# Kernel tuning notes

Measured on AMD Instinct MI355X. Metric: run time of the kernel, lower is better.

The kernel has to match this reference:

```python
import jax, jax.numpy as jnp
import numpy as np

E, T, H, I = 16, 4, 512, 1024  # expert_num, task_num, hidden_size, input_size
B = 8192


def setup_inputs() -> dict:
    key = jax.random.key(0)
    ks = jax.random.split(key, 8)
    s_i = 1.0 / np.sqrt(I)
    s_h = 1.0 / np.sqrt(H)
    return {
        "x": jax.random.normal(ks[0], (B, I), dtype=jnp.float32),
        "We": jax.random.uniform(ks[1], (E, H, I), jnp.float32, -s_i, s_i),
        "be": jax.random.uniform(ks[2], (E, H), jnp.float32, -s_i, s_i),
        "Wg": jax.random.uniform(ks[3], (T, E, I), jnp.float32, -s_i, s_i),
        "bg": jax.random.uniform(ks[4], (T, E), jnp.float32, -s_i, s_i),
        "Wf": jax.random.uniform(ks[5], (T, H), jnp.float32, -s_h, s_h),
        "bf": jax.random.uniform(ks[6], (T,), jnp.float32, -s_h, s_h),
    }


def reference(x, We, be, Wg, bg, Wf, bf):
    # expert outputs: relu(x @ We_e^T + be_e)  -> [B, E, H]
    eo = jax.nn.relu(jnp.einsum("bi,ehi->beh", x, We) + be[None])
    # gate outputs: softmax over experts        -> [B, T, E]
    g = jax.nn.softmax(jnp.einsum("bi,tei->bte", x, Wg) + bg[None], axis=-1)
    # gated combine                             -> [T, B, H]
    res = jnp.einsum("bte,beh->tbh", g, eo)
    # per-task scalar heads                     -> [T, B, 1]
    out = jnp.einsum("tbh,th->tb", res, Wf) + bf[:, None]
    return out[:, :, None]
```

## Files before the change

kernel.cpp:

```cpp
#include <hip/hip_runtime.h>
#include <hip/hip_bf16.h>
#include <stdint.h>


#define E_ 16
#define T_ 4
#define H_ 512
#define I_ 1024
#define B_ 8192
#define N_ (E_ * H_)
#define K_ I_

typedef __bf16 bf16x8 __attribute__((ext_vector_type(8)));
typedef float f32x4 __attribute__((ext_vector_type(4)));

__device__ __forceinline__ unsigned short f2bf_rne(float f) {
  unsigned int b = __float_as_uint(f);
  b += 0x7fffu + ((b >> 16) & 1u);
  return (unsigned short)(b >> 16);
}

#define N4X (B_ * K_ / 4)
#define N4W (N_ * K_ / 4)
#define N4G (64 * K_ / 4)

__global__ __launch_bounds__(256) void cvt3_kernel(const float* __restrict__ x,
                                                   const float* __restrict__ We,
                                                   const float* __restrict__ Wg,
                                                   const float* __restrict__ bfv,
                                                   unsigned short* __restrict__ xb,
                                                   unsigned short* __restrict__ wb,
                                                   unsigned short* __restrict__ wgb,
                                                   float* __restrict__ out) {
  int i = blockIdx.x * 256 + threadIdx.x;
  if (i < T_ * B_) out[i] = bfv[i >> 13];
  const float* src;
  unsigned short* dst;
  int j;
  if (i < N4X) {
    src = x; dst = xb; j = i;
  } else if (i < N4X + N4W) {
    src = We; dst = wb; j = i - N4X;
  } else if (i < N4X + N4W + N4G) {
    src = Wg; dst = wgb; j = i - (N4X + N4W);
  } else {
    return;
  }
  float4 v = reinterpret_cast<const float4*>(src)[j];
  ushort4 o;
  o.x = f2bf_rne(v.x);
  o.y = f2bf_rne(v.y);
  o.z = f2bf_rne(v.z);
  o.w = f2bf_rne(v.w);
  reinterpret_cast<ushort4*>(dst)[j] = o;
}

__device__ __forceinline__ void gld_lds16(const void* gp, void* lp) {
  __builtin_amdgcn_global_load_lds((const __attribute__((address_space(1))) void*)gp,
                                   (__attribute__((address_space(3))) void*)lp, 16, 0, 0);
}

__global__ __launch_bounds__(256) void logits_softmax_kernel(
    const unsigned short* __restrict__ A,
    const unsigned short* __restrict__ Bm,
    const float* __restrict__ bg,
    float* __restrict__ g)
{
  __shared__ struct {
    unsigned short A[128 * 32];
    unsigned short B[64 * 32];
  } st;

  const int tid = threadIdx.x;
  const int w = tid >> 6, l = tid & 63;
  const int m16 = l & 15, q = l >> 4;
  const size_t m0 = (size_t)blockIdx.x * 128;

  const int r0s = (w * 2 + 0) * 16 + (l >> 2);
  const int r1s = (w * 2 + 1) * 16 + (l >> 2);
  const int slot = l & 3;
  const int c0 = slot ^ ((r0s >> 1) & 3);
  const int c1 = slot ^ ((r1s >> 1) & 3);
  const size_t offA0 = (m0 + r0s) * K_ + c0 * 8;
  const size_t offA1 = (m0 + r1s) * K_ + c1 * 8;
  const int l0 = (w * 2 + 0) * 512;
  const int l1 = (w * 2 + 1) * 512;
  const int rBs = w * 16 + (l >> 2);
  const int cB = slot ^ ((rBs >> 1) & 3);
  const size_t offB = (size_t)rBs * K_ + cB * 8;
  const int lB = w * 512;

  const int arow = w * 32 + m16;
  const int sA = q ^ ((arow >> 1) & 3);
  const int sB = q ^ ((m16 >> 1) & 3);

  f32x4 acc[2][4] = {};

  for (int k0 = 0; k0 < K_; k0 += 32) {
    __syncthreads();
    gld_lds16(A + offA0 + k0, st.A + l0);
    gld_lds16(A + offA1 + k0, st.A + l1);
    gld_lds16(Bm + offB + k0, st.B + lB);
    __syncthreads();
    bf16x8 af[2], bfr[4];
#pragma unroll
    for (int i = 0; i < 2; ++i)
      af[i] = *reinterpret_cast<const bf16x8*>(st.A + (arow + i * 16) * 32 + sA * 8);
#pragma unroll
    for (int j = 0; j < 4; ++j)
      bfr[j] = *reinterpret_cast<const bf16x8*>(st.B + (j * 16 + m16) * 32 + sB * 8);
#pragma unroll
    for (int i = 0; i < 2; ++i)
#pragma unroll
      for (int j = 0; j < 4; ++j)
        acc[i][j] = __builtin_amdgcn_mfma_f32_16x16x32_bf16(af[i], bfr[j], acc[i][j], 0, 0, 0);
  }

  float bgv[4];
#pragma unroll
  for (int j = 0; j < 4; ++j) bgv[j] = bg[j * 16 + m16];

#pragma unroll
  for (int i = 0; i < 2; ++i) {
    float lg[4][4];
#pragma unroll
    for (int j = 0; j < 4; ++j)
#pragma unroll
      for (int r = 0; r < 4; ++r) lg[r][j] = acc[i][j][r] + bgv[j];
#pragma unroll
    for (int r = 0; r < 4; ++r) {
#pragma unroll
      for (int j = 0; j < 4; ++j) {
        float m = lg[r][j];
#pragma unroll
        for (int mask = 1; mask < 16; mask <<= 1) m = fmaxf(m, __shfl_xor(m, mask, 64));
        float ex = __expf(lg[r][j] - m);
        float s = ex;
#pragma unroll
        for (int mask = 1; mask < 16; mask <<= 1) s += __shfl_xor(s, mask, 64);
        size_t b = m0 + w * 32 + i * 16 + q * 4 + r;
        g[b * 64 + j * 16 + m16] = ex / s;
      }
    }
  }
}


extern __shared__ char smem[];

#define BARRIER()                          \
  do {                                     \
    asm volatile("" ::: "memory");         \
    __builtin_amdgcn_s_barrier();          \
    asm volatile("" ::: "memory");         \
  } while (0)
#define VMW(n) asm volatile("s_waitcnt vmcnt(" #n ")" ::: "memory")
#define LGKM(n) asm volatile("s_waitcnt lgkmcnt(" #n ")" ::: "memory")
#define SCHED0() __builtin_amdgcn_sched_barrier(0)

#define STAGE4(t_)                                                             \
  do {                                                                         \
    const int bb_ = ((t_) & 3) * 32768;                                        \
    const int ko_ = (t_) * 32;                                                 \
    gld_lds16(A + baseAg + ko_, smem + bb_ + ldsW);                            \
    gld_lds16(A + baseAg + 16 * K_ + ko_, smem + bb_ + ldsW + 1024);           \
    gld_lds16(Bm + baseBg + ko_, smem + bb_ + 16384 + ldsW);                   \
    gld_lds16(Bm + baseBg + 16 * K_ + ko_, smem + bb_ + 16384 + ldsW + 1024);  \
  } while (0)

#define READF(S, t_)                                                                      \
  do {                                                                                    \
    const int bb_ = ((t_) & 3) * 32768;                                                   \
    _Pragma("unroll") for (int i = 0; i < 8; ++i) af##S[i] =                              \
        *reinterpret_cast<const bf16x8*>(smem + bb_ + baseA_rd + i * 1024 + sl16);        \
    _Pragma("unroll") for (int j = 0; j < 4; ++j) bfr##S[j] =                             \
        *reinterpret_cast<const bf16x8*>(smem + bb_ + 16384 + baseB_rd + j * 1024 + sl16);\
  } while (0)

#define MFMA32(S)                                                                         \
  do {                                                                                    \
    __builtin_amdgcn_s_setprio(1);                                                        \
    _Pragma("unroll") for (int i = 0; i < 8; ++i)                                         \
        _Pragma("unroll") for (int j = 0; j < 4; ++j)                                     \
            acc[i][j] = __builtin_amdgcn_mfma_f32_16x16x32_bf16(af##S[i], bfr##S[j],      \
                                                                acc[i][j], 0, 0, 0);      \
    __builtin_amdgcn_s_setprio(0);                                                        \
    SCHED0();                                                                             \
  } while (0)

__global__ __launch_bounds__(512, 2) void moe_main_kernel(
    const unsigned short* __restrict__ A,
    const unsigned short* __restrict__ Bm,
    const float* __restrict__ be,
    const float* __restrict__ Wf,
    const float* __restrict__ g,
    float* __restrict__ out)
{
  const int tid = threadIdx.x;
  const int w = tid >> 6, l = tid & 63;
  const int wm = w >> 2, wn = w & 3;
  const int m16 = l & 15, q = l >> 4;
  const int mb = blockIdx.x, nb = blockIdx.y;
  const size_t m0 = (size_t)mb * 256, n0 = (size_t)nb * 256;

  const int c8 = (((l & 3) ^ ((l >> 3) & 3)) * 8);
  const size_t baseAg = (m0 + w * 32 + (l >> 2)) * K_ + c8;
  const size_t baseBg = (n0 + w * 32 + (l >> 2)) * K_ + c8;
  const int ldsW = w * 2048;

  const int sl16 = (q ^ ((m16 >> 1) & 3)) * 16;
  const int baseA_rd = (wm * 128 + m16) * 64;
  const int baseB_rd = (wn * 64 + m16) * 64;

  f32x4 acc[8][4] = {};
  bf16x8 afA[8], bfrA[4], afB[8], bfrB[4];

  STAGE4(0);
  STAGE4(1);
  STAGE4(2);
  VMW(8);
  BARRIER();
  READF(A, 0);

#pragma unroll 1
  for (int t = 0; t < 28; t += 2) {
    VMW(4);
    BARRIER();
    LGKM(12);
    STAGE4(t + 3);
    READF(B, t + 1);
    LGKM(12);
    SCHED0();
    MFMA32(A);

    VMW(4);
    BARRIER();
    LGKM(12);
    STAGE4(t + 4);
    READF(A, t + 2);
    LGKM(12);
    SCHED0();
    MFMA32(B);
  }
  VMW(4);
  BARRIER();
  LGKM(12);
  STAGE4(31);
  READF(B, 29);
  LGKM(12);
  SCHED0();
  MFMA32(A);
  VMW(4);
  BARRIER();
  READF(A, 30);
  LGKM(12);
  SCHED0();
  MFMA32(B);
  VMW(0);
  BARRIER();
  READF(B, 31);
  LGKM(12);
  SCHED0();
  MFMA32(A);
  LGKM(0);
  SCHED0();
  MFMA32(B);

  __syncthreads();

  float* allsums = (float*)smem;

  const int hb = (int)(n0 & 511);
  const int e_idx = (int)(n0 >> 9);

  float wfv[4][4];
#pragma unroll
  for (int t = 0; t < 4; ++t)
#pragma unroll
    for (int j = 0; j < 4; ++j)
      wfv[t][j] = Wf[t * H_ + hb + wn * 64 + j * 16 + m16];
  float bias[4];
#pragma unroll
  for (int j = 0; j < 4; ++j) bias[j] = be[n0 + wn * 64 + j * 16 + m16];

  const int b0s = m16 & 1, b1s = (m16 >> 1) & 1, b2s = (m16 >> 2) & 1, b3s = (m16 >> 3) & 1;
#pragma unroll
  for (int i = 0; i < 8; ++i) {
    float eo[4][4];
#pragma unroll
    for (int j = 0; j < 4; ++j)
#pragma unroll
      for (int r = 0; r < 4; ++r) eo[j][r] = fmaxf(acc[i][j][r] + bias[j], 0.f);
    float p[16];
#pragma unroll
    for (int r = 0; r < 4; ++r)
#pragma unroll
      for (int t = 0; t < 4; ++t) {
        float v = 0.f;
#pragma unroll
        for (int j = 0; j < 4; ++j) v += eo[j][r] * wfv[t][j];
        p[r * 4 + t] = v;
      }
    float q8[8];
#pragma unroll
    for (int m = 0; m < 8; ++m) {
      float sent = b0s ? p[2 * m] : p[2 * m + 1];
      float recv = __shfl_xor(sent, 1, 64);
      q8[m] = (b0s ? p[2 * m + 1] : p[2 * m]) + recv;
    }
    float q4[4];
#pragma unroll
    for (int u = 0; u < 4; ++u) {
      float sent = b1s ? q8[2 * u] : q8[2 * u + 1];
      float recv = __shfl_xor(sent, 2, 64);
      q4[u] = (b1s ? q8[2 * u + 1] : q8[2 * u]) + recv;
    }
    float q2[2];
#pragma unroll
    for (int u = 0; u < 2; ++u) {
      float sent = b2s ? q4[2 * u] : q4[2 * u + 1];
      float recv = __shfl_xor(sent, 4, 64);
      q2[u] = (b2s ? q4[2 * u + 1] : q4[2 * u]) + recv;
    }
    float sent = b3s ? q2[0] : q2[1];
    float recv = __shfl_xor(sent, 8, 64);
    float v = (b3s ? q2[1] : q2[0]) + recv;

    int row = wm * 128 + i * 16 + q * 4 + (m16 >> 2);
    allsums[wn * 1024 + row * 4 + (m16 & 3)] = v;
  }
  __syncthreads();

  {
    float2 s = *reinterpret_cast<float2*>(&allsums[0 * 1024 + tid * 2]);
    float2 x1 = *reinterpret_cast<float2*>(&allsums[1 * 1024 + tid * 2]);
    float2 x2 = *reinterpret_cast<float2*>(&allsums[2 * 1024 + tid * 2]);
    float2 x3 = *reinterpret_cast<float2*>(&allsums[3 * 1024 + tid * 2]);
    s.x += x1.x + x2.x + x3.x;
    s.y += x1.y + x2.y + x3.y;
#pragma unroll
    for (int oi = 0; oi < 2; ++oi) {
      int o = tid * 2 + oi;
      int row = o >> 2, t = o & 3;
      float sv = oi ? s.y : s.x;
      size_t b = m0 + row;
      float gv = g[b * 64 + t * 16 + e_idx];
      atomicAdd(&out[(size_t)t * B_ + b], gv * sv);
    }
  }
}

extern "C" void kernel_launch(void* const* d_in, const int* in_sizes, int n_in,
                              void* d_out, int out_size, void* d_ws, size_t ws_size,
                              hipStream_t stream) {
  const float* x = (const float*)d_in[0];
  const float* We = (const float*)d_in[1];
  const float* be = (const float*)d_in[2];
  const float* Wg = (const float*)d_in[3];
  const float* bg = (const float*)d_in[4];
  const float* Wf = (const float*)d_in[5];
  const float* bf = (const float*)d_in[6];
  float* out = (float*)d_out;

  unsigned short* xb = (unsigned short*)d_ws;
  unsigned short* wb = xb + (size_t)B_ * K_;
  unsigned short* wgb = wb + (size_t)N_ * K_;
  float* g = (float*)(wgb + (size_t)64 * K_);

  hipFuncSetAttribute((const void*)moe_main_kernel,
                      hipFuncAttributeMaxDynamicSharedMemorySize, 131072);

  cvt3_kernel<<<(N4X + N4W + N4G + 255) / 256, 256, 0, stream>>>(x, We, Wg, bf, xb, wb, wgb, out);
  logits_softmax_kernel<<<B_ / 128, 256, 0, stream>>>(xb, wgb, bg, g);
  dim3 grid(B_ / 256, N_ / 256);
  moe_main_kernel<<<grid, 512, 131072, stream>>>(xb, wb, be, Wf, g, out);
}
```

Measured before the change: 252.6 us.

## Fuse gate logits/softmax into conversion kernel, reading fp32 inputs directly

Merges the fp32-to-bf16 conversion kernel and the gate logits/softmax kernel into one launch. The first 64 blocks compute gate logits straight from fp32 x and Wg, converting to bf16 in registers and staging through double-buffered LDS with register prefetch. The remaining blocks convert x and We and initialise the output. This removes one kernel launch and the dependency on a pre-converted Wg. The gate blocks now read fp32 x, so they move twice the bytes, and the bf16 packing is done per tile inside the loop.

```diff
diff --git a/kernel.cpp b/kernel.cpp
--- a/kernel.cpp
+++ b/kernel.cpp
@@ -22,93 +22,115 @@
 
 #define N4X (B_ * K_ / 4)
 #define N4W (N_ * K_ / 4)
-#define N4G (64 * K_ / 4)
-
-__global__ __launch_bounds__(256) void cvt3_kernel(const float* __restrict__ x,
-                                                   const float* __restrict__ We,
-                                                   const float* __restrict__ Wg,
-                                                   const float* __restrict__ bfv,
-                                                   unsigned short* __restrict__ xb,
-                                                   unsigned short* __restrict__ wb,
-                                                   unsigned short* __restrict__ wgb,
-                                                   float* __restrict__ out) {
-  int i = blockIdx.x * 256 + threadIdx.x;
-  if (i < T_ * B_) out[i] = bfv[i >> 13];
-  const float* src;
-  unsigned short* dst;
-  int j;
-  if (i < N4X) {
-    src = x; dst = xb; j = i;
-  } else if (i < N4X + N4W) {
-    src = We; dst = wb; j = i - N4X;
-  } else if (i < N4X + N4W + N4G) {
-    src = Wg; dst = wgb; j = i - (N4X + N4W);
-  } else {
-    return;
-  }
-  float4 v = reinterpret_cast<const float4*>(src)[j];
-  ushort4 o;
-  o.x = f2bf_rne(v.x);
-  o.y = f2bf_rne(v.y);
-  o.z = f2bf_rne(v.z);
-  o.w = f2bf_rne(v.w);
-  reinterpret_cast<ushort4*>(dst)[j] = o;
-}
 
 __device__ __forceinline__ void gld_lds16(const void* gp, void* lp) {
   __builtin_amdgcn_global_load_lds((const __attribute__((address_space(1))) void*)gp,
                                    (__attribute__((address_space(3))) void*)lp, 16, 0, 0);
 }
 
-__global__ __launch_bounds__(256) void logits_softmax_kernel(
-    const unsigned short* __restrict__ A,
-    const unsigned short* __restrict__ Bm,
+__global__ __launch_bounds__(256) void prep_kernel(
+    const float* __restrict__ x,
+    const float* __restrict__ Wg,
     const float* __restrict__ bg,
-    float* __restrict__ g)
+    const float* __restrict__ We,
+    const float* __restrict__ bfv,
+    unsigned short* __restrict__ xb,
+    unsigned short* __restrict__ wb,
+    float* __restrict__ g,
+    float* __restrict__ out)
 {
+  const int tid = threadIdx.x;
+
+  if (blockIdx.x >= 64) {
+    int i = (blockIdx.x - 64) * 256 + tid;
+    if (i < T_ * B_) out[i] = bfv[i >> 13];
+    const float* src;
+    unsigned short* dst;
+    int j;
+    if (i < N4X) {
+      src = x; dst = xb; j = i;
+    } else if (i < N4X + N4W) {
+      src = We; dst = wb; j = i - N4X;
+    } else {
+      return;
+    }
+    float4 v = reinterpret_cast<const float4*>(src)[j];
+    ushort4 o;
+    o.x = f2bf_rne(v.x);
+    o.y = f2bf_rne(v.y);
+    o.z = f2bf_rne(v.z);
+    o.w = f2bf_rne(v.w);
+    reinterpret_cast<ushort4*>(dst)[j] = o;
+    return;
+  }
+
   __shared__ struct {
-    unsigned short A[128 * 32];
-    unsigned short B[64 * 32];
+    unsigned short A[2][128 * 32];
+    unsigned short B[2][64 * 32];
   } st;
 
-  const int tid = threadIdx.x;
   const int w = tid >> 6, l = tid & 63;
   const int m16 = l & 15, q = l >> 4;
   const size_t m0 = (size_t)blockIdx.x * 128;
 
-  const int r0s = (w * 2 + 0) * 16 + (l >> 2);
-  const int r1s = (w * 2 + 1) * 16 + (l >> 2);
-  const int slot = l & 3;
-  const int c0 = slot ^ ((r0s >> 1) & 3);
-  const int c1 = slot ^ ((r1s >> 1) & 3);
-  const size_t offA0 = (m0 + r0s) * K_ + c0 * 8;
-  const size_t offA1 = (m0 + r1s) * K_ + c1 * 8;
-  const int l0 = (w * 2 + 0) * 512;
-  const int l1 = (w * 2 + 1) * 512;
-  const int rBs = w * 16 + (l >> 2);
-  const int cB = slot ^ ((rBs >> 1) & 3);
-  const size_t offB = (size_t)rBs * K_ + cB * 8;
-  const int lB = w * 512;
+  const int ra = tid >> 1, kh = tid & 1;
+  const float* xrow = x + (m0 + ra) * K_ + kh * 16;
+  const float* grow = Wg + (size_t)ra * K_ + kh * 16;
+  const int swA0 = ((kh * 2 + 0) ^ ((ra >> 1) & 3)) * 8;
+  const int swA1 = ((kh * 2 + 1) ^ ((ra >> 1) & 3)) * 8;
 
   const int arow = w * 32 + m16;
   const int sA = q ^ ((arow >> 1) & 3);
   const int sB = q ^ ((m16 >> 1) & 3);
 
+  float4 apf0, apf1, apf2, apf3, bpf0, bpf1, bpf2, bpf3;
+#define LOADREG(kt_)                                                    \
+  do {                                                                  \
+    const float4* xp = reinterpret_cast<const float4*>(xrow + (kt_) * 32); \
+    apf0 = xp[0]; apf1 = xp[1]; apf2 = xp[2]; apf3 = xp[3];             \
+    if (tid < 128) {                                                    \
+      const float4* gp = reinterpret_cast<const float4*>(grow + (kt_) * 32); \
+      bpf0 = gp[0]; bpf1 = gp[1]; bpf2 = gp[2]; bpf3 = gp[3];           \
+    }                                                                   \
+  } while (0)
+
+#define PACK8(dst_, va_, vb_)                                           \
+  do {                                                                  \
+    union { ushort u[8]; uint4 v; } pk_;                                \
+    pk_.u[0] = f2bf_rne(va_.x); pk_.u[1] = f2bf_rne(va_.y);             \
+    pk_.u[2] = f2bf_rne(va_.z); pk_.u[3] = f2bf_rne(va_.w);             \
+    pk_.u[4] = f2bf_rne(vb_.x); pk_.u[5] = f2bf_rne(vb_.y);             \
+    pk_.u[6] = f2bf_rne(vb_.z); pk_.u[7] = f2bf_rne(vb_.w);             \
+    *reinterpret_cast<uint4*>(dst_) = pk_.v;                            \
+  } while (0)
+
+#define WRITE_LDS(pb_)                                                  \
+  do {                                                                  \
+    PACK8(st.A[pb_] + ra * 32 + swA0, apf0, apf1);                      \
+    PACK8(st.A[pb_] + ra * 32 + swA1, apf2, apf3);                      \
+    if (tid < 128) {                                                    \
+      PACK8(st.B[pb_] + ra * 32 + swA0, bpf0, bpf1);                    \
+      PACK8(st.B[pb_] + ra * 32 + swA1, bpf2, bpf3);                    \
+    }                                                                   \
+  } while (0)
+
   f32x4 acc[2][4] = {};
 
-  for (int k0 = 0; k0 < K_; k0 += 32) {
+  LOADREG(0);
+#pragma unroll 1
+  for (int kt = 0; kt < 32; ++kt) {
+    const int pb = kt & 1;
     __syncthreads();
-    gld_lds16(A + offA0 + k0, st.A + l0);
-    gld_lds16(A + offA1 + k0, st.A + l1);
-    gld_lds16(Bm + offB + k0, st.B + lB);
+    WRITE_LDS(pb);
+    if (kt < 31) LOADREG(kt + 1);
     __syncthreads();
     bf16x8 af[2], bfr[4];
 #pragma unroll
     for (int i = 0; i < 2; ++i)
-      af[i] = *reinterpret_cast<const bf16x8*>(st.A + (arow + i * 16) * 32 + sA * 8);
+      af[i] = *reinterpret_cast<const bf16x8*>(st.A[pb] + (arow + i * 16) * 32 + sA * 8);
 #pragma unroll
     for (int j = 0; j < 4; ++j)
-      bfr[j] = *reinterpret_cast<const bf16x8*>(st.B + (j * 16 + m16) * 32 + sB * 8);
+      bfr[j] = *reinterpret_cast<const bf16x8*>(st.B[pb] + (j * 16 + m16) * 32 + sB * 8);
 #pragma unroll
     for (int i = 0; i < 2; ++i)
 #pragma unroll
@@ -364,14 +386,12 @@
 
   unsigned short* xb = (unsigned short*)d_ws;
   unsigned short* wb = xb + (size_t)B_ * K_;
-  unsigned short* wgb = wb + (size_t)N_ * K_;
-  float* g = (float*)(wgb + (size_t)64 * K_);
+  float* g = (float*)(wb + (size_t)N_ * K_);
 
   hipFuncSetAttribute((const void*)moe_main_kernel,
                       hipFuncAttributeMaxDynamicSharedMemorySize, 131072);
 
-  cvt3_kernel<<<(N4X + N4W + N4G + 255) / 256, 256, 0, stream>>>(x, We, Wg, bf, xb, wb, wgb, out);
-  logits_softmax_kernel<<<B_ / 128, 256, 0, stream>>>(xb, wgb, bg, g);
+  prep_kernel<<<64 + (N4X + N4W) / 256, 256, 0, stream>>>(x, Wg, bg, We, bf, xb, wb, g, out);
   dim3 grid(B_ / 256, N_ / 256);
   moe_main_kernel<<<grid, 512, 131072, stream>>>(xb, wb, be, Wf, g, out);
 }
```

After: 257.3 us. About the same (+1.9%).
